# Kernel tuning notes

Measured on AMD Instinct MI355X. Metric: run time of the kernel, lower is better.

Reference implementation:

```python
import jax, jax.numpy as jnp
import numpy as np

B, N_IN, O, IN_L, OUT_L = 256, 1152, 10, 8, 16
ITERS = 3
EPS = 1e-7

def squash(s, eps):
    # norm over the capsule-length axis (-2), keepdim, as in the torch code
    dot = jnp.sum(s * s, axis=-2, keepdims=True)
    return (dot / (1.0 + dot) / jnp.sqrt(dot + eps)) * s

def setup_inputs() -> dict:
    key = jax.random.key(0)
    k1, k2, k3 = jax.random.split(key, 3)
    x = jax.random.normal(k1, (B, N_IN, IN_L, 1), dtype=jnp.float32)
    weight = 0.05 * jax.random.normal(k2, (1, N_IN, O, IN_L, OUT_L), dtype=jnp.float32)
    bias = 0.05 * jax.random.normal(k3, (1, 1, O, OUT_L, 1), dtype=jnp.float32)
    return {"x": x, "weight": weight, "bias": bias}

def reference(x, weight, bias):
    # u_hat[b,n,o,k] = sum_i W[0,n,o,i,k] * x[b,n,i,0]  -> (B, N, O, K, 1)
    u_hat = jnp.einsum('noik,bni->bnok', weight[0], x[..., 0])[..., None]
    u_det = jax.lax.stop_gradient(u_hat)
    b_ij = jnp.zeros((x.shape[0], N_IN, O, 1, 1), dtype=x.dtype)
    v = None
    for r in range(ITERS):
        c = jax.nn.softmax(b_ij, axis=2)          # routing coefficients over out caps
        u = u_hat if r == ITERS - 1 else u_det    # detached except last iter
        s = jnp.sum(c * u, axis=1, keepdims=True) + bias  # (B,1,O,K,1)
        v = squash(s, EPS)
        if r != ITERS - 1:
            # agreement: sum over capsule-length axis 3 -> (B,N,O,1,1)
            b_ij = b_ij + jnp.sum(u_det * v, axis=3, keepdims=True)
    return v
```

## Files before the change

kernel.cpp:

```cpp
#include <hip/hip_runtime.h>
#include <hip/hip_bf16.h>

#define BB   256
#define NIN  1152
#define OO   10
#define IL   8
#define OL   16
#define ROW  (OO*OL)
#define EPSQ 1e-7f
#define NTT  16
#define BT2  16
#define NCH2 (NIN/NTT)

typedef unsigned short ushx8 __attribute__((ext_vector_type(8)));

__device__ __forceinline__ float bf2f(unsigned short h) {
    unsigned u = ((unsigned)h) << 16;
    return __builtin_bit_cast(float, u);
}

__global__ __launch_bounds__(320) void caps_build2(
    const float* __restrict__ x, const float* __restrict__ w,
    unsigned short* __restrict__ u, float* __restrict__ psum)
{
    __shared__ float4 wl4[4][330];
    const int t    = threadIdx.x;
    const int bloc = t / 20;
    const int oct  = t - bloc * 20;
    const int o    = oct >> 1;
    const int k8   = oct & 1;
    const int n0   = blockIdx.x * NTT;
    const int b    = blockIdx.y * BT2 + bloc;

    const int so = t >> 5;
    const int sr = t & 31;
    const int si = sr >> 2;
    const int sk = sr & 3;
    const int sdst = so * 33 + si * 4 + sk;

    const float* xb = x + ((size_t)b * NIN + n0) * 8;
    unsigned short* ub = u + ((size_t)b * NIN + n0) * ROW + o * OL + k8 * 8;

    float ps[8];
    #pragma unroll
    for (int j = 0; j < 8; ++j) ps[j] = 0.f;

    for (int sub = 0; sub < 4; ++sub) {
        __syncthreads();
        const float4* wg = reinterpret_cast<const float4*>(w)
                         + (size_t)(n0 + sub * 4) * 320;
        #pragma unroll
        for (int jj = 0; jj < 4; ++jj)
            wl4[jj][sdst] = wg[jj * 320 + t];
        __syncthreads();

        #pragma unroll
        for (int nn = 0; nn < 4; ++nn) {
            const int nrel = sub * 4 + nn;
            const float4 x0 = *reinterpret_cast<const float4*>(xb + nrel * 8);
            const float4 x1 = *reinterpret_cast<const float4*>(xb + nrel * 8 + 4);
            const float xv[IL] = {x0.x, x0.y, x0.z, x0.w, x1.x, x1.y, x1.z, x1.w};

            float acc[8];
            #pragma unroll
            for (int j = 0; j < 8; ++j) acc[j] = 0.f;

            const float4* wbase = &wl4[nn][o * 33 + k8 * 2];
            #pragma unroll
            for (int i = 0; i < IL; ++i) {
                const float4 wlo = wbase[i * 4];
                const float4 whi = wbase[i * 4 + 1];
                acc[0] = fmaf(wlo.x, xv[i], acc[0]);
                acc[1] = fmaf(wlo.y, xv[i], acc[1]);
                acc[2] = fmaf(wlo.z, xv[i], acc[2]);
                acc[3] = fmaf(wlo.w, xv[i], acc[3]);
                acc[4] = fmaf(whi.x, xv[i], acc[4]);
                acc[5] = fmaf(whi.y, xv[i], acc[5]);
                acc[6] = fmaf(whi.z, xv[i], acc[6]);
                acc[7] = fmaf(whi.w, xv[i], acc[7]);
            }

            union { ushx8 v; __hip_bfloat162 h[4]; } pk;
            #pragma unroll
            for (int j = 0; j < 4; ++j)
                pk.h[j] = __float22bfloat162_rn(make_float2(acc[2*j], acc[2*j+1]));
            *reinterpret_cast<ushx8*>(ub + (size_t)nrel * ROW) = pk.v;

            #pragma unroll
            for (int j = 0; j < 8; ++j) ps[j] += acc[j];
        }
    }

    float* pp = psum + ((size_t)blockIdx.x * BB + b) * ROW + oct * 8;
    *reinterpret_cast<float4*>(pp)     = make_float4(ps[0], ps[1], ps[2], ps[3]);
    *reinterpret_cast<float4*>(pp + 4) = make_float4(ps[4], ps[5], ps[6], ps[7]);
}

__global__ __launch_bounds__(192) void caps_squash0(
    const float* __restrict__ psum, const float* __restrict__ bias,
    float* __restrict__ v0)
{
    const int t = threadIdx.x;
    if (t >= ROW) return;
    const int b = blockIdx.x;

    float s0 = 0.f, s1 = 0.f, s2 = 0.f, s3 = 0.f;
    const float* pt = psum + (size_t)b * ROW + t;
    #pragma unroll
    for (int ch = 0; ch < NCH2; ch += 4) {
        s0 += pt[(size_t)(ch + 0) * BB * ROW];
        s1 += pt[(size_t)(ch + 1) * BB * ROW];
        s2 += pt[(size_t)(ch + 2) * BB * ROW];
        s3 += pt[(size_t)(ch + 3) * BB * ROW];
    }
    const float s = 0.1f * ((s0 + s1) + (s2 + s3)) + bias[t];

    float d = s * s;
    d += __shfl_xor(d, 1, 16);
    d += __shfl_xor(d, 2, 16);
    d += __shfl_xor(d, 4, 16);
    d += __shfl_xor(d, 8, 16);
    const float f = d / ((1.f + d) * sqrtf(d + EPSQ));
    v0[(size_t)b * ROW + t] = f * s;
}

__global__ __launch_bounds__(768) void caps_route2(
    const unsigned short* __restrict__ u, const float* __restrict__ bias,
    const float* __restrict__ v0g, float* __restrict__ outv)
{
    __shared__ float lds[12][ROW];
    __shared__ float vbuf[ROW];
    const int t  = threadIdx.x;
    const int q  = t & 3;
    const int g  = t >> 2;
    const int wv = t >> 6;
    const int b  = blockIdx.x;
    const unsigned short* ub = u + (size_t)b * NIN * ROW;

    float bsv = 0.f;
    float vprev = 0.f;
    if (t < ROW) {
        bsv = bias[t];
        const float v = v0g[(size_t)b * ROW + t];
        vbuf[t] = v;
        vprev = v;
    }
    __syncthreads();

    #pragma unroll
    for (int iter = 1; iter < 3; ++iter) {
        float sp[5][8];
        #pragma unroll
        for (int j = 0; j < 5; ++j)
            #pragma unroll
            for (int e = 0; e < 8; ++e) sp[j][e] = 0.f;

        float vs[5][8];
        #pragma unroll
        for (int j = 0; j < 5; ++j) {
            #pragma unroll
            for (int e = 0; e < 8; ++e) vs[j][e] = vbuf[(q + 4 * j) * 8 + e];
        }

        for (int m = 0; m < 6; ++m) {
            const unsigned short* un = ub + (size_t)(g + m * 192) * ROW;
            float uf[5][8];
            #pragma unroll
            for (int j = 0; j < 5; ++j) {
                const ushx8 raw = *reinterpret_cast<const ushx8*>(un + (q + 4 * j) * 8);
                #pragma unroll
                for (int e = 0; e < 8; ++e) uf[j][e] = bf2f(raw[e]);
            }

            float d[5], dd[5];
            #pragma unroll
            for (int j = 0; j < 5; ++j) {
                float acc = uf[j][0] * vs[j][0];
                #pragma unroll
                for (int e = 1; e < 8; ++e) acc = fmaf(uf[j][e], vs[j][e], acc);
                acc += __shfl_xor(acc, 1, 4);
                d[j] = acc;
            }
            #pragma unroll
            for (int j = 0; j < 5; ++j) dd[j] = __shfl_xor(d[j], 2, 4);

            float mx = fmaxf(d[0], dd[0]);
            #pragma unroll
            for (int j = 1; j < 5; ++j) mx = fmaxf(mx, fmaxf(d[j], dd[j]));
            float se = 0.f, e_[5];
            #pragma unroll
            for (int j = 0; j < 5; ++j) {
                e_[j] = __expf(d[j] - mx);
                se += e_[j] + __expf(dd[j] - mx);
            }
            const float r = 1.f / se;
            #pragma unroll
            for (int j = 0; j < 5; ++j) {
                const float c = e_[j] * r;
                #pragma unroll
                for (int e = 0; e < 8; ++e)
                    sp[j][e] = fmaf(c, uf[j][e], sp[j][e]);
            }
        }

        #pragma unroll
        for (int j = 0; j < 5; ++j)
            #pragma unroll
            for (int e = 0; e < 8; ++e) {
                #pragma unroll
                for (int msk = 4; msk <= 32; msk <<= 1)
                    sp[j][e] += __shfl_xor(sp[j][e], msk);
            }
        if ((t & 63) < 4) {
            #pragma unroll
            for (int j = 0; j < 5; ++j)
                #pragma unroll
                for (int e = 0; e < 8; ++e)
                    lds[wv][(q + 4 * j) * 8 + e] = sp[j][e];
        }
        __syncthreads();

        if (t < ROW) {
            float ssum = 0.f;
            #pragma unroll
            for (int wvi = 0; wvi < 12; ++wvi) ssum += lds[wvi][t];
            const float sv = ssum + bsv;

            float dq = sv * sv;
            dq += __shfl_xor(dq, 1, 16);
            dq += __shfl_xor(dq, 2, 16);
            dq += __shfl_xor(dq, 4, 16);
            dq += __shfl_xor(dq, 8, 16);
            const float f = dq / ((1.f + dq) * sqrtf(dq + EPSQ));
            const float v = f * sv;

            if (iter == 1) { vbuf[t] = v + vprev; }
            else           { outv[(size_t)b * ROW + t] = v; }
        }
        __syncthreads();
    }
}

extern "C" void kernel_launch(void* const* d_in, const int* in_sizes, int n_in,
                              void* d_out, int out_size, void* d_ws, size_t ws_size,
                              hipStream_t stream) {
    const float* x    = (const float*)d_in[0];
    const float* w    = (const float*)d_in[1];
    const float* bias = (const float*)d_in[2];
    float* out = (float*)d_out;

    unsigned short* u = (unsigned short*)d_ws;
    float* psum = (float*)((char*)d_ws + (size_t)BB * NIN * ROW * 2);
    float* v0   = psum + (size_t)NCH2 * BB * ROW;

    caps_build2<<<dim3(NIN / NTT, BB / BT2), 320, 0, stream>>>(x, w, u, psum);
    caps_squash0<<<BB, 192, 0, stream>>>(psum, bias, v0);
    caps_route2<<<BB, 768, 0, stream>>>(u, bias, v0, out);
}
```

Measured before the change: 81.81 us.

## Keep weights in registers and reduce partial sums across n in LDS

The build kernel is restructured so each thread owns one input capsule n and holds its weight slice in registers, then loops over 16 batch rows instead of reloading weights from LDS per n. Partial sums over the 8 n's in a block are reduced through shared memory per batch row. The tile shape changes from 16 n × 16 b to 8 n × 32 b, which doubles the psum chunk count, and squash0 is adjusted to read more chunks. The cost is two block-wide barriers per batch row and more psum traffic. The u stores also become strided across n per thread, which may weaken write coalescing.

```diff
diff --git a/kernel.cpp b/kernel.cpp
--- a/kernel.cpp
+++ b/kernel.cpp
@@ -8,9 +8,9 @@
 #define OL   16
 #define ROW  (OO*OL)
 #define EPSQ 1e-7f
-#define NTT  16
-#define BT2  16
-#define NCH2 (NIN/NTT)
+#define NT4  8
+#define BT4  32
+#define NCH2 (NIN/NT4)
 
 typedef unsigned short ushx8 __attribute__((ext_vector_type(8)));
 
@@ -19,81 +19,99 @@
     return __builtin_bit_cast(float, u);
 }
 
-__global__ __launch_bounds__(320) void caps_build2(
+__global__ __launch_bounds__(320, 1) void caps_build4(
     const float* __restrict__ x, const float* __restrict__ w,
     unsigned short* __restrict__ u, float* __restrict__ psum)
 {
-    __shared__ float4 wl4[4][330];
-    const int t    = threadIdx.x;
-    const int bloc = t / 20;
-    const int oct  = t - bloc * 20;
-    const int o    = oct >> 1;
-    const int k8   = oct & 1;
-    const int n0   = blockIdx.x * NTT;
-    const int b    = blockIdx.y * BT2 + bloc;
-
-    const int so = t >> 5;
-    const int sr = t & 31;
-    const int si = sr >> 2;
-    const int sk = sr & 3;
-    const int sdst = so * 33 + si * 4 + sk;
-
-    const float* xb = x + ((size_t)b * NIN + n0) * 8;
-    unsigned short* ub = u + ((size_t)b * NIN + n0) * ROW + o * OL + k8 * 8;
-
-    float ps[8];
-    #pragma unroll
-    for (int j = 0; j < 8; ++j) ps[j] = 0.f;
-
-    for (int sub = 0; sub < 4; ++sub) {
-        __syncthreads();
-        const float4* wg = reinterpret_cast<const float4*>(w)
-                         + (size_t)(n0 + sub * 4) * 320;
-        #pragma unroll
-        for (int jj = 0; jj < 4; ++jj)
+    __shared__ float4 wl4[NT4][331];
+    __shared__ float4 redA[8][40];
+    __shared__ float4 redB[8][40];
+    const int t   = threadIdx.x;
+    const int nl  = t & 7;
+    const int r   = t >> 3;
+    const int hh  = r / 20;
+    const int oct = r - hh * 20;
+    const int o   = oct >> 1;
+    const int k8  = oct & 1;
+    const int n0  = blockIdx.x * NT4;
+    const int b0  = blockIdx.y * BT4;
+    const int n   = n0 + nl;
+
+    {
+        const float4* wg = reinterpret_cast<const float4*>(w) + (size_t)n0 * 320;
+        const int so = t >> 5;
+        const int si = (t >> 2) & 7;
+        const int sk = t & 3;
+        const int sdst = so * 33 + si * 4 + sk;
+        #pragma unroll
+        for (int jj = 0; jj < 8; ++jj)
             wl4[jj][sdst] = wg[jj * 320 + t];
-        __syncthreads();
-
-        #pragma unroll
-        for (int nn = 0; nn < 4; ++nn) {
-            const int nrel = sub * 4 + nn;
-            const float4 x0 = *reinterpret_cast<const float4*>(xb + nrel * 8);
-            const float4 x1 = *reinterpret_cast<const float4*>(xb + nrel * 8 + 4);
-            const float xv[IL] = {x0.x, x0.y, x0.z, x0.w, x1.x, x1.y, x1.z, x1.w};
-
-            float acc[8];
-            #pragma unroll
-            for (int j = 0; j < 8; ++j) acc[j] = 0.f;
-
-            const float4* wbase = &wl4[nn][o * 33 + k8 * 2];
-            #pragma unroll
-            for (int i = 0; i < IL; ++i) {
-                const float4 wlo = wbase[i * 4];
-                const float4 whi = wbase[i * 4 + 1];
-                acc[0] = fmaf(wlo.x, xv[i], acc[0]);
-                acc[1] = fmaf(wlo.y, xv[i], acc[1]);
-                acc[2] = fmaf(wlo.z, xv[i], acc[2]);
-                acc[3] = fmaf(wlo.w, xv[i], acc[3]);
-                acc[4] = fmaf(whi.x, xv[i], acc[4]);
-                acc[5] = fmaf(whi.y, xv[i], acc[5]);
-                acc[6] = fmaf(whi.z, xv[i], acc[6]);
-                acc[7] = fmaf(whi.w, xv[i], acc[7]);
-            }
-
-            union { ushx8 v; __hip_bfloat162 h[4]; } pk;
-            #pragma unroll
-            for (int j = 0; j < 4; ++j)
-                pk.h[j] = __float22bfloat162_rn(make_float2(acc[2*j], acc[2*j+1]));
-            *reinterpret_cast<ushx8*>(ub + (size_t)nrel * ROW) = pk.v;
-
-            #pragma unroll
-            for (int j = 0; j < 8; ++j) ps[j] += acc[j];
-        }
-    }
-
-    float* pp = psum + ((size_t)blockIdx.x * BB + b) * ROW + oct * 8;
-    *reinterpret_cast<float4*>(pp)     = make_float4(ps[0], ps[1], ps[2], ps[3]);
-    *reinterpret_cast<float4*>(pp + 4) = make_float4(ps[4], ps[5], ps[6], ps[7]);
+    }
+    __syncthreads();
+
+    float4 wlo[IL], whi[IL];
+    {
+        const float4* wbase = &wl4[nl][o * 33 + k8 * 2];
+        #pragma unroll
+        for (int i = 0; i < IL; ++i) {
+            wlo[i] = wbase[i * 4];
+            whi[i] = wbase[i * 4 + 1];
+        }
+    }
+
+    const float4* xg = reinterpret_cast<const float4*>(x);
+    unsigned short* ub = u + ((size_t)(b0 + hh * 16) * NIN + n) * ROW
+                           + o * OL + k8 * 8;
+    const size_t ustride = (size_t)NIN * ROW;
+
+    for (int bl = 0; bl < 16; ++bl) {
+        const int b = b0 + hh * 16 + bl;
+        const float4 x0 = xg[((size_t)b * NIN + n) * 2];
+        const float4 x1 = xg[((size_t)b * NIN + n) * 2 + 1];
+        const float xv[IL] = {x0.x, x0.y, x0.z, x0.w, x1.x, x1.y, x1.z, x1.w};
+
+        float acc[8];
+        #pragma unroll
+        for (int j = 0; j < 8; ++j) acc[j] = 0.f;
+        #pragma unroll
+        for (int i = 0; i < IL; ++i) {
+            acc[0] = fmaf(wlo[i].x, xv[i], acc[0]);
+            acc[1] = fmaf(wlo[i].y, xv[i], acc[1]);
+            acc[2] = fmaf(wlo[i].z, xv[i], acc[2]);
+            acc[3] = fmaf(wlo[i].w, xv[i], acc[3]);
+            acc[4] = fmaf(whi[i].x, xv[i], acc[4]);
+            acc[5] = fmaf(whi[i].y, xv[i], acc[5]);
+            acc[6] = fmaf(whi[i].z, xv[i], acc[6]);
+            acc[7] = fmaf(whi[i].w, xv[i], acc[7]);
+        }
+
+        union { ushx8 v; __hip_bfloat162 h[4]; } pk;
+        #pragma unroll
+        for (int j = 0; j < 4; ++j)
+            pk.h[j] = __float22bfloat162_rn(make_float2(acc[2*j], acc[2*j+1]));
+        *reinterpret_cast<ushx8*>(ub + (size_t)bl * ustride) = pk.v;
+
+        redA[nl][r] = make_float4(acc[0], acc[1], acc[2], acc[3]);
+        redB[nl][r] = make_float4(acc[4], acc[5], acc[6], acc[7]);
+        __syncthreads();
+
+        if (t < 40) {
+            float4 sA = redA[0][t], sB = redB[0][t];
+            #pragma unroll
+            for (int n2 = 1; n2 < 8; ++n2) {
+                const float4 a = redA[n2][t], bv = redB[n2][t];
+                sA.x += a.x;  sA.y += a.y;  sA.z += a.z;  sA.w += a.w;
+                sB.x += bv.x; sB.y += bv.y; sB.z += bv.z; sB.w += bv.w;
+            }
+            const int hh2  = t / 20;
+            const int oct2 = t - hh2 * 20;
+            float* pp = psum + ((size_t)blockIdx.x * BB + b0 + hh2 * 16 + bl) * ROW
+                             + oct2 * 8;
+            *reinterpret_cast<float4*>(pp)     = sA;
+            *reinterpret_cast<float4*>(pp + 4) = sB;
+        }
+        __syncthreads();
+    }
 }
 
 __global__ __launch_bounds__(192) void caps_squash0(
@@ -104,24 +122,25 @@
     if (t >= ROW) return;
     const int b = blockIdx.x;
 
-    float s0 = 0.f, s1 = 0.f, s2 = 0.f, s3 = 0.f;
+    float s[8];
+    #pragma unroll
+    for (int j = 0; j < 8; ++j) s[j] = 0.f;
     const float* pt = psum + (size_t)b * ROW + t;
-    #pragma unroll
-    for (int ch = 0; ch < NCH2; ch += 4) {
-        s0 += pt[(size_t)(ch + 0) * BB * ROW];
-        s1 += pt[(size_t)(ch + 1) * BB * ROW];
-        s2 += pt[(size_t)(ch + 2) * BB * ROW];
-        s3 += pt[(size_t)(ch + 3) * BB * ROW];
-    }
-    const float s = 0.1f * ((s0 + s1) + (s2 + s3)) + bias[t];
-
-    float d = s * s;
+    for (int ch = 0; ch < NCH2; ch += 8) {
+        #pragma unroll
+        for (int j = 0; j < 8; ++j)
+            s[j] += pt[(size_t)(ch + j) * BB * ROW];
+    }
+    const float ssum = ((s[0]+s[1]) + (s[2]+s[3])) + ((s[4]+s[5]) + (s[6]+s[7]));
+    const float sv = 0.1f * ssum + bias[t];
+
+    float d = sv * sv;
     d += __shfl_xor(d, 1, 16);
     d += __shfl_xor(d, 2, 16);
     d += __shfl_xor(d, 4, 16);
     d += __shfl_xor(d, 8, 16);
     const float f = d / ((1.f + d) * sqrtf(d + EPSQ));
-    v0[(size_t)b * ROW + t] = f * s;
+    v0[(size_t)b * ROW + t] = f * sv;
 }
 
 __global__ __launch_bounds__(768) void caps_route2(
@@ -193,10 +212,10 @@
                 e_[j] = __expf(d[j] - mx);
                 se += e_[j] + __expf(dd[j] - mx);
             }
-            const float r = 1.f / se;
-            #pragma unroll
-            for (int j = 0; j < 5; ++j) {
-                const float c = e_[j] * r;
+            const float rr = 1.f / se;
+            #pragma unroll
+            for (int j = 0; j < 5; ++j) {
+                const float c = e_[j] * rr;
                 #pragma unroll
                 for (int e = 0; e < 8; ++e)
                     sp[j][e] = fmaf(c, uf[j][e], sp[j][e]);
@@ -253,7 +272,7 @@
     float* psum = (float*)((char*)d_ws + (size_t)BB * NIN * ROW * 2);
     float* v0   = psum + (size_t)NCH2 * BB * ROW;
 
-    caps_build2<<<dim3(NIN / NTT, BB / BT2), 320, 0, stream>>>(x, w, u, psum);
+    caps_build4<<<dim3(NIN / NT4, BB / BT4), 320, 0, stream>>>(x, w, u, psum);
     caps_squash0<<<BB, 192, 0, stream>>>(psum, bias, v0);
     caps_route2<<<BB, 768, 0, stream>>>(u, bias, v0, out);
 }
```

Result: slower. 105.6 us (+29.1%).
